# Kernel tuning notes

Hardware: AMD Instinct MI355X
Metric: run time of the kernel (lower is better)

The kernel has to match this reference:

```python
import jax, jax.numpy as jnp
import numpy as np

B, T, C = 4, 2048, 1024
H = 16
D = C // H  # head_dim = 64


def setup_inputs() -> dict:
    key = jax.random.key(0)
    ks = jax.random.split(key, 6)
    s = 1.0 / np.sqrt(C)
    x = jax.random.normal(ks[0], (B, T, C), dtype=jnp.float32)
    Wq = jax.random.normal(ks[1], (C, C), dtype=jnp.float32) * s
    Wk = jax.random.normal(ks[2], (C, C), dtype=jnp.float32) * s
    Wv = jax.random.normal(ks[3], (C, C), dtype=jnp.float32) * s
    Wo = jax.random.normal(ks[4], (C, C), dtype=jnp.float32) * s
    bo = jnp.zeros((C,), dtype=jnp.float32)
    # causal mask, 1 = attend, 0 = masked (masked_fill(mask==0, -inf))
    mask = jnp.broadcast_to(jnp.tril(jnp.ones((T, T), dtype=jnp.int32)), (B, T, T))
    return {"x": x, "mask": mask, "Wq": Wq, "Wk": Wk, "Wv": Wv, "Wo": Wo, "bo": bo}


def reference(x, mask, Wq, Wk, Wv, Wo, bo):
    Bx, Tx, Cx = x.shape
    # projections; nn.Linear computes x @ W.T, here W is stored as (C, C) applied as x @ W
    Q = (x @ Wq).reshape(Bx, Tx, H, D).transpose(0, 2, 1, 3)  # (B,H,T,D)
    K = (x @ Wk).reshape(Bx, Tx, H, D).transpose(0, 2, 1, 3)
    V = (x @ Wv).reshape(Bx, Tx, H, D).transpose(0, 2, 1, 3)
    scores = jnp.einsum('bhqd,bhkd->bhqk', Q, K) / jnp.sqrt(jnp.float32(D))
    scores = jnp.where(mask[:, None, :, :] == 0, -jnp.inf, scores)
    attn = jax.nn.softmax(scores, axis=-1)
    ctx = jnp.einsum('bhqk,bhkd->bhqd', attn, V)  # (B,H,T,D)
    ctx = ctx.transpose(0, 2, 1, 3).reshape(Bx, Tx, Cx)
    return ctx @ Wo + bo
```

## Files before the change

### kernel.cpp

```cpp
#include <hip/hip_runtime.h>
#include <hip/hip_bf16.h>


#define B_  4
#define T_  2048
#define C_  1024
#define H_  16
#define D_  64
#define M_  (B_*T_)

#define LOG2E 1.4426950408889634f

using bf16x8 = __attribute__((ext_vector_type(8))) short;
using f32x4  = __attribute__((ext_vector_type(4))) float;
using u16x4  = __attribute__((ext_vector_type(4))) unsigned short;

__device__ __forceinline__ unsigned short f2bf(float f) {
  union { float f; unsigned u; } cv; cv.f = f;
  unsigned u = cv.u;
  u += 0x7fffu + ((u >> 16) & 1u);
  return (unsigned short)(u >> 16);
}

__device__ __forceinline__ unsigned cvt_pk_bf16(float lo, float hi) {
  unsigned r;
  asm("v_cvt_pk_bf16_f32 %0, %1, %2" : "=v"(r) : "v"(lo), "v"(hi));
  return r;
}

__device__ __forceinline__ float exp2fast(float x) {
#if __has_builtin(__builtin_amdgcn_exp2f)
  return __builtin_amdgcn_exp2f(x);
#else
  return exp2f(x);
#endif
}

__device__ __forceinline__ void lds_load16(void* lds, const void* g) {
  __builtin_amdgcn_global_load_lds(
      (const __attribute__((address_space(1))) unsigned int*)g,
      (__attribute__((address_space(3))) unsigned int*)lds,
      16, 0, 0);
}

__global__ __launch_bounds__(256) void conv_x_kernel(
    const float* __restrict__ x, unsigned short* __restrict__ xb) {
  int i = blockIdx.x * 256 + threadIdx.x;
  const float4* xv = (const float4*)x;
  float4 a = xv[i * 2 + 0];
  float4 b = xv[i * 2 + 1];
  using u16x8 = __attribute__((ext_vector_type(8))) unsigned short;
  u16x8 o;
  o[0]=f2bf(a.x); o[1]=f2bf(a.y); o[2]=f2bf(a.z); o[3]=f2bf(a.w);
  o[4]=f2bf(b.x); o[5]=f2bf(b.y); o[6]=f2bf(b.z); o[7]=f2bf(b.w);
  *(u16x8*)&xb[(size_t)i * 8] = o;
}

__global__ __launch_bounds__(256) void conv_wt_kernel(
    const float* __restrict__ W0, const float* __restrict__ W1,
    const float* __restrict__ W2, const float* __restrict__ W3,
    unsigned short* __restrict__ WT) {
  __shared__ float tile[64][65];
  const float* W = (blockIdx.z == 0) ? W0 : (blockIdx.z == 1) ? W1
                 : (blockIdx.z == 2) ? W2 : W3;
  unsigned short* o = WT + (size_t)blockIdx.z * C_ * C_;
  const int k0 = blockIdx.y * 64, n0 = blockIdx.x * 64;
  const int tr = threadIdx.x >> 6;
  const int tc = threadIdx.x & 63;
#pragma unroll
  for (int i = 0; i < 16; ++i) {
    int k = tr + i * 4;
    tile[k][tc] = W[(size_t)(k0 + k) * C_ + n0 + tc];
  }
  __syncthreads();
#pragma unroll
  for (int i = 0; i < 16; ++i) {
    int n = tr + i * 4;
    o[(size_t)(n0 + n) * C_ + k0 + tc] = f2bf(tile[tc][n]);
  }
}

template <int EPI>
__global__ __launch_bounds__(256) void gemm128(
    const unsigned short* __restrict__ A, const unsigned short* __restrict__ BT,
    void* __restrict__ out, const float* __restrict__ bias, int K) {
  __shared__ unsigned short As[128][32];
  __shared__ unsigned short Bs[128][32];

  const int tid  = threadIdx.x;
  const int wid  = tid >> 6, lane = tid & 63;
  const int wr   = wid >> 1, wc = wid & 1;
  const int fr   = lane & 15, fq = lane >> 4;
  const int bm   = blockIdx.y, bn = blockIdx.x;

  const unsigned short* aP = A  + (size_t)(bm * 128 + wid * 32 + (lane >> 2)) * K + (lane & 3) * 8;
  const unsigned short* bP = BT + (size_t)(bn * 128 + wid * 32 + (lane >> 2)) * K + (lane & 3) * 8;
  unsigned short* asB = &As[wid * 32][0];
  unsigned short* bsB = &Bs[wid * 32][0];

  f32x4 acc[4][4] = {};

  for (int k0 = 0; k0 < K; k0 += 32) {
    lds_load16(asB,           aP + k0);
    lds_load16(asB + 16 * 32, aP + (size_t)16 * K + k0);
    lds_load16(bsB,           bP + k0);
    lds_load16(bsB + 16 * 32, bP + (size_t)16 * K + k0);
    __syncthreads();

    bf16x8 af[4], bfr[4];
#pragma unroll
    for (int mi = 0; mi < 4; ++mi)
      af[mi] = *(const bf16x8*)&As[wr * 64 + mi * 16 + fr][fq * 8];
#pragma unroll
    for (int ni = 0; ni < 4; ++ni)
      bfr[ni] = *(const bf16x8*)&Bs[wc * 64 + ni * 16 + fr][fq * 8];
#pragma unroll
    for (int mi = 0; mi < 4; ++mi)
#pragma unroll
      for (int ni = 0; ni < 4; ++ni)
        acc[mi][ni] = __builtin_amdgcn_mfma_f32_16x16x32_bf16(
            af[mi], bfr[ni], acc[mi][ni], 0, 0, 0);
    __syncthreads();
  }

  if (EPI == 0) {
    unsigned short* o = (unsigned short*)out;
#pragma unroll
    for (int mi = 0; mi < 4; ++mi) {
      int m  = bm * 128 + wr * 64 + mi * 16 + fq * 4;
      int b  = m >> 11;
      int t0 = m & 2047;
#pragma unroll
      for (int ni = 0; ni < 4; ++ni) {
        int n = bn * 128 + wc * 64 + ni * 16 + fr;
        int mat = n >> 10;
        int nc  = n & 1023;
        int h = nc >> 6, d = nc & 63;
        float sc_ = (mat == 0) ? (0.125f * LOG2E) : 1.0f;
        size_t base = (size_t)mat * ((size_t)M_ * C_) + ((size_t)(b * H_ + h) << 17) + d;
#pragma unroll
        for (int r = 0; r < 4; ++r)
          o[base + (size_t)(t0 + r) * D_] = f2bf(acc[mi][ni][r] * sc_);
      }
    }
  } else {
    float* o = (float*)out;
#pragma unroll
    for (int mi = 0; mi < 4; ++mi) {
      int m = bm * 128 + wr * 64 + mi * 16 + fq * 4;
#pragma unroll
      for (int ni = 0; ni < 4; ++ni) {
        int n = bn * 128 + wc * 64 + ni * 16 + fr;
        float bv = bias[n];
#pragma unroll
        for (int r = 0; r < 4; ++r)
          o[(size_t)(m + r) * C_ + n] = acc[mi][ni][r] + bv;
      }
    }
  }
}

#define KSTR 72
__global__ __launch_bounds__(256) void attn_kernel(
    const unsigned short* __restrict__ Qg, const unsigned short* __restrict__ Kg,
    const unsigned short* __restrict__ Vg, unsigned short* __restrict__ ctx) {
  __shared__ __align__(16) unsigned short Ks[64][KSTR];
  __shared__ __align__(16) unsigned short VTs[64][KSTR];
  __shared__ __align__(16) unsigned short Ps[4][2][16][KSTR];

  const int tid = threadIdx.x, wid = tid >> 6, lane = tid & 63;
  const int fr = lane & 15, fq = lane >> 4;

  const int bid = blockIdx.x;
  const int xcd = bid & 7, j = bid >> 3;
  const int bh = xcd * 8 + (j & 7);
  const int pA = j >> 3;
  const int b = bh >> 4, h = bh & 15;
  const size_t base = (size_t)bh * (T_ * D_);

  const int ksr = tid >> 2, ksc = tid & 3;
  const unsigned short* Kptr = Kg + base + (size_t)ksr * D_ + ksc * 8;
  const int vc = tid >> 5, vr_ = tid & 31;
  const unsigned short* Vptr = Vg + base + (size_t)(2 * vr_) * D_ + vc * 8;

  int4 kr0, kr1, va, vb;
  auto stage_load = [&](int kv) {
    const unsigned short* kp = Kptr + (size_t)kv * D_;
    kr0 = *(const int4*)kp;
    kr1 = *(const int4*)(kp + 32);
    const unsigned short* vp = Vptr + (size_t)kv * D_;
    va = *(const int4*)vp;
    vb = *(const int4*)(vp + D_);
  };
  auto stage_write = [&]() {
    *(int4*)&Ks[ksr][ksc * 8]       = kr0;
    *(int4*)&Ks[ksr][(ksc + 4) * 8] = kr1;
    const unsigned short* pa = (const unsigned short*)&va;
    const unsigned short* pb = (const unsigned short*)&vb;
#pragma unroll
    for (int i = 0; i < 8; ++i) {
      unsigned w = (unsigned)pa[i] | ((unsigned)pb[i] << 16);
      *(unsigned*)&VTs[vc * 8 + i][2 * vr_] = w;
    }
  };

  stage_load(0);
  stage_write();

  int seg = 0;
  int qbase = pA * 128;

  bf16x8 qf[2][2];
  auto qload = [&]() {
#pragma unroll
    for (int x = 0; x < 2; ++x)
#pragma unroll
      for (int t = 0; t < 2; ++t)
        qf[x][t] = *(const bf16x8*)
            &Qg[base + (size_t)(qbase + 64 * x + wid * 16 + fr) * D_ + t * 32 + fq * 8];
  };
  qload();

  f32x4 acc[2][4] = {};
  float m_run[2] = {-__builtin_inff(), -__builtin_inff()};
  float l_run[2] = {0.f, 0.f};

  int kv0 = 0;
  for (int s = 0; s < 34; ++s) {
    const bool lastof    = (kv0 == qbase + 64);
    const bool have_next = !(lastof && seg == 1);
    const int  nkv = lastof ? 0 : kv0 + 64;

    __syncthreads();
    if (have_next) stage_load(nkv);

    bf16x8 kf[8];
#pragma unroll
    for (int nt = 0; nt < 4; ++nt)
#pragma unroll
      for (int t = 0; t < 2; ++t)
        kf[nt * 2 + t] = *(const bf16x8*)&Ks[nt * 16 + fr][t * 32 + fq * 8];

#pragma unroll
    for (int x = 0; x < 2; ++x) {
      f32x4 sv[4];
      __builtin_amdgcn_s_setprio(1);
#pragma unroll
      for (int nt = 0; nt < 4; ++nt) {
        f32x4 sa = {};
        sa = __builtin_amdgcn_mfma_f32_16x16x32_bf16(kf[nt * 2 + 0], qf[x][0], sa, 0, 0, 0);
        sa = __builtin_amdgcn_mfma_f32_16x16x32_bf16(kf[nt * 2 + 1], qf[x][1], sa, 0, 0, 0);
        sv[nt] = sa;
      }
      __builtin_amdgcn_s_setprio(0);

      float mt = -__builtin_inff();
      if (kv0 >= qbase + 64 * x) {
        const int qi = qbase + 64 * x + wid * 16 + fr;
#pragma unroll
        for (int nt = 0; nt < 4; ++nt)
#pragma unroll
          for (int r = 0; r < 4; ++r) {
            int kvi = kv0 + nt * 16 + fq * 4 + r;
            float v = sv[nt][r];
            if (kvi > qi) v = -__builtin_inff();
            sv[nt][r] = v;
            mt = fmaxf(mt, v);
          }
      } else {
#pragma unroll
        for (int nt = 0; nt < 4; ++nt)
#pragma unroll
          for (int r = 0; r < 4; ++r) mt = fmaxf(mt, sv[nt][r]);
      }
      mt = fmaxf(mt, __shfl_xor(mt, 16));
      mt = fmaxf(mt, __shfl_xor(mt, 32));

      {
        float mn = fmaxf(m_run[x], mt);
        float c  = (mn == m_run[x]) ? 1.0f : exp2fast(m_run[x] - mn);
        m_run[x] = mn;
#pragma unroll
        for (int dt = 0; dt < 4; ++dt) acc[x][dt] *= c;
        l_run[x] *= c;
      }

      float lsum = 0.f;
#pragma unroll
      for (int nt = 0; nt < 4; ++nt) {
        float p0 = exp2fast(sv[nt][0] - m_run[x]);
        float p1 = exp2fast(sv[nt][1] - m_run[x]);
        float p2 = exp2fast(sv[nt][2] - m_run[x]);
        float p3 = exp2fast(sv[nt][3] - m_run[x]);
        lsum += (p0 + p1) + (p2 + p3);
        uint2 pk;
        pk.x = cvt_pk_bf16(p0, p1);
        pk.y = cvt_pk_bf16(p2, p3);
        *(uint2*)&Ps[wid][x][fr][nt * 16 + fq * 4] = pk;
      }
      lsum += __shfl_xor(lsum, 16);
      lsum += __shfl_xor(lsum, 32);
      l_run[x] += lsum;
    }

    __builtin_amdgcn_s_setprio(1);
#pragma unroll
    for (int t = 0; t < 2; ++t) {
      bf16x8 pf0 = *(const bf16x8*)&Ps[wid][0][fr][t * 32 + fq * 8];
      bf16x8 pf1 = *(const bf16x8*)&Ps[wid][1][fr][t * 32 + fq * 8];
#pragma unroll
      for (int dt = 0; dt < 4; ++dt) {
        bf16x8 vf = *(const bf16x8*)&VTs[dt * 16 + fr][t * 32 + fq * 8];
        acc[0][dt] = __builtin_amdgcn_mfma_f32_16x16x32_bf16(vf, pf0, acc[0][dt], 0, 0, 0);
        acc[1][dt] = __builtin_amdgcn_mfma_f32_16x16x32_bf16(vf, pf1, acc[1][dt], 0, 0, 0);
      }
    }
    __builtin_amdgcn_s_setprio(0);

    __syncthreads();
    if (have_next) stage_write();

    if (lastof) {
#pragma unroll
      for (int x = 0; x < 2; ++x) {
        float linv = 1.0f / l_run[x];
        unsigned short* orow =
            ctx + (size_t)(b * T_ + qbase + 64 * x + wid * 16 + fr) * C_ + h * D_;
#pragma unroll
        for (int dt = 0; dt < 4; ++dt) {
          u16x4 o;
#pragma unroll
          for (int r = 0; r < 4; ++r) o[r] = f2bf(acc[x][dt][r] * linv);
          *(u16x4*)&orow[dt * 16 + fq * 4] = o;
        }
      }
      if (seg == 0) {
        seg = 1; qbase = (15 - pA) * 128;
        qload();
#pragma unroll
        for (int x = 0; x < 2; ++x) {
#pragma unroll
          for (int dt = 0; dt < 4; ++dt) acc[x][dt] = f32x4{0.f, 0.f, 0.f, 0.f};
          m_run[x] = -__builtin_inff();
          l_run[x] = 0.f;
        }
        kv0 = 0;
      }
    } else {
      kv0 += 64;
    }
  }
}

extern "C" void kernel_launch(void* const* d_in, const int* in_sizes, int n_in,
                              void* d_out, int out_size, void* d_ws, size_t ws_size,
                              hipStream_t stream) {
  const float* x  = (const float*)d_in[0];
  const float* Wq = (const float*)d_in[2];
  const float* Wk = (const float*)d_in[3];
  const float* Wv = (const float*)d_in[4];
  const float* Wo = (const float*)d_in[5];
  const float* bo = (const float*)d_in[6];

  unsigned short* xb  = (unsigned short*)d_ws;
  unsigned short* wqt = xb  + (size_t)M_ * C_;
  unsigned short* wot = wqt + (size_t)3 * C_ * C_;
  unsigned short* Qb  = wot + (size_t)C_ * C_;
  unsigned short* ctxb = xb;

  conv_x_kernel<<<4096, 256, 0, stream>>>(x, xb);
  conv_wt_kernel<<<dim3(16, 16, 4), 256, 0, stream>>>(Wq, Wk, Wv, Wo, wqt);

  gemm128<0><<<dim3(24, M_ / 128), 256, 0, stream>>>(xb, wqt, Qb, nullptr, C_);

  attn_kernel<<<dim3(512), 256, 0, stream>>>(
      Qb, Qb + (size_t)M_ * C_, Qb + (size_t)2 * M_ * C_, ctxb);

  gemm128<1><<<dim3(8, M_ / 128), 256, 0, stream>>>(ctxb, wot, d_out, bo, C_);
}
```

Measured before the change: 203.5 us.

## Split paired causal query tiles into separate blocks, heaviest-first launch order

Replaces the scheme where each block processed two complementary 128-row query tiles (pA and 15-pA) back to back with one query tile per block, doubling the grid to 1024 blocks. Block index is mapped so the longest causal tiles (qt=15 down) are scheduled first, relying on the hardware scheduler for load balance instead of manual pairing. This removes the mid-loop segment switch and reload logic but gives up the guaranteed equal work per block, and adds per-block startup overhead and a more uneven tail.

```diff
diff --git a/kernel.cpp b/kernel.cpp
--- a/kernel.cpp
+++ b/kernel.cpp
@@ -174,7 +174,7 @@
   const int bid = blockIdx.x;
   const int xcd = bid & 7, j = bid >> 3;
   const int bh = xcd * 8 + (j & 7);
-  const int pA = j >> 3;
+  const int qt = 15 - (j >> 3);
   const int b = bh >> 4, h = bh & 15;
   const size_t base = (size_t)bh * (T_ * D_);
 
@@ -207,32 +207,27 @@
   stage_load(0);
   stage_write();
 
-  int seg = 0;
-  int qbase = pA * 128;
+  const int qbase = qt * 128;
 
   bf16x8 qf[2][2];
-  auto qload = [&]() {
-#pragma unroll
-    for (int x = 0; x < 2; ++x)
-#pragma unroll
-      for (int t = 0; t < 2; ++t)
-        qf[x][t] = *(const bf16x8*)
-            &Qg[base + (size_t)(qbase + 64 * x + wid * 16 + fr) * D_ + t * 32 + fq * 8];
-  };
-  qload();
+#pragma unroll
+  for (int x = 0; x < 2; ++x)
+#pragma unroll
+    for (int t = 0; t < 2; ++t)
+      qf[x][t] = *(const bf16x8*)
+          &Qg[base + (size_t)(qbase + 64 * x + wid * 16 + fr) * D_ + t * 32 + fq * 8];
 
   f32x4 acc[2][4] = {};
   float m_run[2] = {-__builtin_inff(), -__builtin_inff()};
   float l_run[2] = {0.f, 0.f};
 
+  const int nsteps = 2 * qt + 2;
   int kv0 = 0;
-  for (int s = 0; s < 34; ++s) {
-    const bool lastof    = (kv0 == qbase + 64);
-    const bool have_next = !(lastof && seg == 1);
-    const int  nkv = lastof ? 0 : kv0 + 64;
+  for (int s = 0; s < nsteps; ++s) {
+    const bool have_next = (s + 1 < nsteps);
 
     __syncthreads();
-    if (have_next) stage_load(nkv);
+    if (have_next) stage_load(kv0 + 64);
 
     bf16x8 kf[8];
 #pragma unroll
@@ -320,34 +315,20 @@
     __syncthreads();
     if (have_next) stage_write();
 
-    if (lastof) {
-#pragma unroll
-      for (int x = 0; x < 2; ++x) {
-        float linv = 1.0f / l_run[x];
-        unsigned short* orow =
-            ctx + (size_t)(b * T_ + qbase + 64 * x + wid * 16 + fr) * C_ + h * D_;
-#pragma unroll
-        for (int dt = 0; dt < 4; ++dt) {
-          u16x4 o;
-#pragma unroll
-          for (int r = 0; r < 4; ++r) o[r] = f2bf(acc[x][dt][r] * linv);
-          *(u16x4*)&orow[dt * 16 + fq * 4] = o;
-        }
-      }
-      if (seg == 0) {
-        seg = 1; qbase = (15 - pA) * 128;
-        qload();
-#pragma unroll
-        for (int x = 0; x < 2; ++x) {
-#pragma unroll
-          for (int dt = 0; dt < 4; ++dt) acc[x][dt] = f32x4{0.f, 0.f, 0.f, 0.f};
-          m_run[x] = -__builtin_inff();
-          l_run[x] = 0.f;
-        }
-        kv0 = 0;
-      }
-    } else {
-      kv0 += 64;
+    kv0 += 64;
+  }
+
+#pragma unroll
+  for (int x = 0; x < 2; ++x) {
+    float linv = 1.0f / l_run[x];
+    unsigned short* orow =
+        ctx + (size_t)(b * T_ + qbase + 64 * x + wid * 16 + fr) * C_ + h * D_;
+#pragma unroll
+    for (int dt = 0; dt < 4; ++dt) {
+      u16x4 o;
+#pragma unroll
+      for (int r = 0; r < 4; ++r) o[r] = f2bf(acc[x][dt][r] * linv);
+      *(u16x4*)&orow[dt * 16 + fq * 4] = o;
     }
   }
 }
@@ -373,7 +354,7 @@
 
   gemm128<0><<<dim3(24, M_ / 128), 256, 0, stream>>>(xb, wqt, Qb, nullptr, C_);
 
-  attn_kernel<<<dim3(512), 256, 0, stream>>>(
+  attn_kernel<<<dim3(1024), 256, 0, stream>>>(
       Qb, Qb + (size_t)M_ * C_, Qb + (size_t)2 * M_ * C_, ctxb);
 
   gemm128<1><<<dim3(8, M_ / 128), 256, 0, stream>>>(ctxb, wot, d_out, bo, C_);
```

New measurement: 204.4 us. No clear change (+0.4%).
